# Performance work log

Hardware: AMD Instinct MI355X
Metric: run time of the kernel (lower is better)

The kernel has to match this reference:

```python
import jax, jax.numpy as jnp
import numpy as np

B, C, F, N = 2, 8, 80, 128
H, W = 512, 1024


def setup_inputs() -> dict:
    key = jax.random.key(0)
    k1, k2, k3 = jax.random.split(key, 3)
    x = jax.random.normal(k1, (B, C, F, N, N), dtype=jnp.float32)
    quad = jax.random.randint(k2, (H, W), 0, F, dtype=jnp.int32)
    # uv buffer holds coordinates already scaled into [0, N-1]
    uv = jax.random.uniform(k3, (H, W, 2), dtype=jnp.float32) * (N - 1)
    return {"x": x, "quad": quad, "uv": uv}


def reference(x, quad, uv):
    """x: B x C x F x N x N texture patches; quad: H x W face indices;
    uv: H x W x 2 in-patch coordinates in [0, N-1]. Returns B x C x H x W."""
    Bx, Cx, Fx, Nx, _ = x.shape
    Hh, Ww = quad.shape
    u = uv[..., 0].reshape(-1)  # HW
    v = uv[..., 1].reshape(-1)
    u0 = jnp.clip(jnp.floor(u), 0, Nx - 2).astype(jnp.int32)
    v0 = jnp.clip(jnp.floor(v), 0, Nx - 2).astype(jnp.int32)
    du = u - u0.astype(u.dtype)
    dv = v - v0.astype(v.dtype)
    base = quad.reshape(-1).astype(jnp.int32) * (Nx * Nx)  # HW
    x_flat = x.reshape(Bx, Cx, Fx * Nx * Nx)
    i00 = base + v0 * Nx + u0
    g00 = x_flat[:, :, i00]           # B x C x HW
    g01 = x_flat[:, :, i00 + 1]
    g10 = x_flat[:, :, i00 + Nx]
    g11 = x_flat[:, :, i00 + Nx + 1]
    w00 = (1.0 - du) * (1.0 - dv)
    w01 = du * (1.0 - dv)
    w10 = (1.0 - du) * dv
    w11 = du * dv
    out = g00 * w00 + g01 * w01 + g10 * w10 + g11 * w11  # B x C x HW
    return out.reshape(Bx, Cx, Hh, Ww)
```

## Files before the change

### kernel.cpp

```cpp
#include <hip/hip_runtime.h>
#include <hip/hip_fp16.h>

#define BC   16
#define FD   80
#define ND   128
#define NN   (ND * ND)
#define HW   (512 * 1024)
#define HW_SHIFT 19

#define YH_BYTES ((size_t)FD * NN * BC * sizeof(__half))

__global__ __launch_bounds__(256)
void repack_kernel(const float* __restrict__ x, __half* __restrict__ y)
{
    const int fv = blockIdx.x;
    const int f  = fv / ND;
    const int v  = fv - f * ND;
    const int tid = threadIdx.x;

    __shared__ float lds[ND * 17];

#pragma unroll
    for (int i = tid; i < BC * ND; i += 256) {
        const int bc = i >> 7;
        const int u  = i & (ND - 1);
        lds[u * 17 + bc] = x[(((size_t)bc * FD + f) * ND + v) * ND + u];
    }
    __syncthreads();

    const int u  = tid >> 1;
    const int c0 = (tid & 1) * 8;
    uint4 r;
    unsigned* rp = (unsigned*)&r;
#pragma unroll
    for (int j = 0; j < 4; ++j) {
        const __half2 h = __floats2half2_rn(lds[u * 17 + c0 + 2 * j],
                                            lds[u * 17 + c0 + 2 * j + 1]);
        rp[j] = *(const unsigned*)&h;
    }
    uint4* y4 = (uint4*)(y + (size_t)fv * ND * BC);
    y4[tid] = r;
}

__device__ inline float4 loadh4(const __half* p)
{
    const __half2* q = (const __half2*)p;
    const float2 fa = __half22float2(q[0]);
    const float2 fb = __half22float2(q[1]);
    return make_float4(fa.x, fa.y, fb.x, fb.y);
}

__global__ __launch_bounds__(256)
void gather_kernel(const __half* __restrict__ y,
                   const int*    __restrict__ quad,
                   const float2* __restrict__ uv2,
                   float* __restrict__ out)
{
    const int gid = blockIdx.x * 256 + threadIdx.x;
    const int pix = gid >> 2;
    const int bc0 = (gid & 3) * 4;

    const float2 t = uv2[pix];
    const int    f = quad[pix];

    const float u = t.x;
    const float v = t.y;

    int u0 = (int)floorf(u);
    int v0 = (int)floorf(v);
    u0 = min(max(u0, 0), ND - 2);
    v0 = min(max(v0, 0), ND - 2);

    const float du = u - (float)u0;
    const float dv = v - (float)v0;

    const float w00 = (1.0f - du) * (1.0f - dv);
    const float w01 = du * (1.0f - dv);
    const float w10 = (1.0f - du) * dv;
    const float w11 = du * dv;

    const size_t base = (((size_t)f * ND + v0) * ND + u0) * BC + bc0;
    const float4 g00 = loadh4(y + base);
    const float4 g01 = loadh4(y + base + BC);
    const float4 g10 = loadh4(y + base + (size_t)ND * BC);
    const float4 g11 = loadh4(y + base + (size_t)ND * BC + BC);

    const float o0 = g00.x * w00 + g01.x * w01 + g10.x * w10 + g11.x * w11;
    const float o1 = g00.y * w00 + g01.y * w01 + g10.y * w10 + g11.y * w11;
    const float o2 = g00.z * w00 + g01.z * w01 + g10.z * w10 + g11.z * w11;
    const float o3 = g00.w * w00 + g01.w * w01 + g10.w * w10 + g11.w * w11;

    __builtin_nontemporal_store(o0, &out[(size_t)(bc0 + 0) * HW + pix]);
    __builtin_nontemporal_store(o1, &out[(size_t)(bc0 + 1) * HW + pix]);
    __builtin_nontemporal_store(o2, &out[(size_t)(bc0 + 2) * HW + pix]);
    __builtin_nontemporal_store(o3, &out[(size_t)(bc0 + 3) * HW + pix]);
}

__global__ __launch_bounds__(256)
void resample_fallback_kernel(const float* __restrict__ x,
                              const int*   __restrict__ quad,
                              const float2* __restrict__ uv2,
                              float* __restrict__ out)
{
    const int gid = blockIdx.x * 256 + threadIdx.x;
    const int pix = gid & (HW - 1);
    const int bc  = gid >> HW_SHIFT;

    const float2 t = uv2[pix];
    const int    f = quad[pix];

    const float u = t.x;
    const float v = t.y;

    int u0 = (int)floorf(u);
    int v0 = (int)floorf(v);
    u0 = min(max(u0, 0), ND - 2);
    v0 = min(max(v0, 0), ND - 2);

    const float du = u - (float)u0;
    const float dv = v - (float)v0;

    const float w00 = (1.0f - du) * (1.0f - dv);
    const float w01 = du * (1.0f - dv);
    const float w10 = (1.0f - du) * dv;
    const float w11 = du * dv;

    const float* p = x + ((size_t)bc * FD + (size_t)f) * NN + v0 * ND + u0;
    out[gid] = p[0] * w00 + p[1] * w01 + p[ND] * w10 + p[ND + 1] * w11;
}

extern "C" void kernel_launch(void* const* d_in, const int* in_sizes, int n_in,
                              void* d_out, int out_size, void* d_ws, size_t ws_size,
                              hipStream_t stream)
{
    const float*  x    = (const float*)d_in[0];
    const int*    quad = (const int*)d_in[1];
    const float2* uv2  = (const float2*)d_in[2];
    float*        out  = (float*)d_out;

    if (ws_size >= YH_BYTES) {
        __half* y = (__half*)d_ws;
        repack_kernel<<<FD * ND, 256, 0, stream>>>(x, y);
        const int total = 4 * HW;
        gather_kernel<<<total / 256, 256, 0, stream>>>(y, quad, uv2, out);
    } else {
        const int total = BC * HW;
        resample_fallback_kernel<<<total / 256, 256, 0, stream>>>(x, quad, uv2, out);
    }
}
```

Baseline: 170.0 us.

## Gather all 16 channels per thread with wide loads; vectorize repack reads

```diff
diff --git a/kernel.cpp b/kernel.cpp
--- a/kernel.cpp
+++ b/kernel.cpp
@@ -13,18 +13,24 @@
 __global__ __launch_bounds__(256)
 void repack_kernel(const float* __restrict__ x, __half* __restrict__ y)
 {
-    const int fv = blockIdx.x;
-    const int f  = fv / ND;
-    const int v  = fv - f * ND;
+    const int fv  = blockIdx.x;
+    const int f   = fv >> 7;
+    const int v   = fv & (ND - 1);
     const int tid = threadIdx.x;
 
     __shared__ float lds[ND * 17];
 
 #pragma unroll
-    for (int i = tid; i < BC * ND; i += 256) {
-        const int bc = i >> 7;
-        const int u  = i & (ND - 1);
-        lds[u * 17 + bc] = x[(((size_t)bc * FD + f) * ND + v) * ND + u];
+    for (int r = 0; r < 2; ++r) {
+        const int i4 = tid + r * 256;
+        const int c  = i4 >> 5;
+        const int u4 = i4 & 31;
+        const float4 val = *(const float4*)(
+            x + (((size_t)c * FD + f) * ND + v) * ND + u4 * 4);
+        lds[(u4 * 4 + 0) * 17 + c] = val.x;
+        lds[(u4 * 4 + 1) * 17 + c] = val.y;
+        lds[(u4 * 4 + 2) * 17 + c] = val.z;
+        lds[(u4 * 4 + 3) * 17 + c] = val.w;
     }
     __syncthreads();
 
@@ -42,12 +48,15 @@
     y4[tid] = r;
 }
 
-__device__ inline float4 loadh4(const __half* p)
+__device__ inline void acc8(float* o, uint4 t, float w)
 {
-    const __half2* q = (const __half2*)p;
-    const float2 fa = __half22float2(q[0]);
-    const float2 fb = __half22float2(q[1]);
-    return make_float4(fa.x, fa.y, fb.x, fb.y);
+    const unsigned* p = (const unsigned*)&t;
+#pragma unroll
+    for (int j = 0; j < 4; ++j) {
+        const float2 fp = __half22float2(*(const __half2*)&p[j]);
+        o[2 * j + 0] += fp.x * w;
+        o[2 * j + 1] += fp.y * w;
+    }
 }
 
 __global__ __launch_bounds__(256)
@@ -56,9 +65,7 @@
                    const float2* __restrict__ uv2,
                    float* __restrict__ out)
 {
-    const int gid = blockIdx.x * 256 + threadIdx.x;
-    const int pix = gid >> 2;
-    const int bc0 = (gid & 3) * 4;
+    const int pix = blockIdx.x * 256 + threadIdx.x;
 
     const float2 t = uv2[pix];
     const int    f = quad[pix];
@@ -71,29 +78,33 @@
     u0 = min(max(u0, 0), ND - 2);
     v0 = min(max(v0, 0), ND - 2);
 
+    const size_t base = (((size_t)f * ND + v0) * ND + u0) * BC;
+    const uint4* r0 = (const uint4*)(y + base);
+    const uint4* r1 = (const uint4*)(y + base + (size_t)ND * BC);
+    const uint4 a0 = r0[0], a1 = r0[1];
+    const uint4 b0 = r0[2], b1 = r0[3];
+    const uint4 c0 = r1[0], c1 = r1[1];
+    const uint4 d0 = r1[2], d1 = r1[3];
+
     const float du = u - (float)u0;
     const float dv = v - (float)v0;
-
     const float w00 = (1.0f - du) * (1.0f - dv);
     const float w01 = du * (1.0f - dv);
     const float w10 = (1.0f - du) * dv;
     const float w11 = du * dv;
 
-    const size_t base = (((size_t)f * ND + v0) * ND + u0) * BC + bc0;
-    const float4 g00 = loadh4(y + base);
-    const float4 g01 = loadh4(y + base + BC);
-    const float4 g10 = loadh4(y + base + (size_t)ND * BC);
-    const float4 g11 = loadh4(y + base + (size_t)ND * BC + BC);
+    float o[BC];
+#pragma unroll
+    for (int c = 0; c < BC; ++c) o[c] = 0.0f;
 
-    const float o0 = g00.x * w00 + g01.x * w01 + g10.x * w10 + g11.x * w11;
-    const float o1 = g00.y * w00 + g01.y * w01 + g10.y * w10 + g11.y * w11;
-    const float o2 = g00.z * w00 + g01.z * w01 + g10.z * w10 + g11.z * w11;
-    const float o3 = g00.w * w00 + g01.w * w01 + g10.w * w10 + g11.w * w11;
+    acc8(o,     a0, w00); acc8(o + 8, a1, w00);
+    acc8(o,     b0, w01); acc8(o + 8, b1, w01);
+    acc8(o,     c0, w10); acc8(o + 8, c1, w10);
+    acc8(o,     d0, w11); acc8(o + 8, d1, w11);
 
-    __builtin_nontemporal_store(o0, &out[(size_t)(bc0 + 0) * HW + pix]);
-    __builtin_nontemporal_store(o1, &out[(size_t)(bc0 + 1) * HW + pix]);
-    __builtin_nontemporal_store(o2, &out[(size_t)(bc0 + 2) * HW + pix]);
-    __builtin_nontemporal_store(o3, &out[(size_t)(bc0 + 3) * HW + pix]);
+#pragma unroll
+    for (int c = 0; c < BC; ++c)
+        __builtin_nontemporal_store(o[c], &out[(size_t)c * HW + pix]);
 }
 
 __global__ __launch_bounds__(256)
@@ -141,8 +152,7 @@
     if (ws_size >= YH_BYTES) {
         __half* y = (__half*)d_ws;
         repack_kernel<<<FD * ND, 256, 0, stream>>>(x, y);
-        const int total = 4 * HW;
-        gather_kernel<<<total / 256, 256, 0, stream>>>(y, quad, uv2, out);
+        gather_kernel<<<HW / 256, 256, 0, stream>>>(y, quad, uv2, out);
     } else {
         const int total = BC * HW;
         resample_fallback_kernel<<<total / 256, 256, 0, stream>>>(x, quad, uv2, out);
```

Result: no change. 167.2 us (-1.7%).
